# Kernel tuning notes

Measured on AMD Instinct MI355X. Metric: run time of the kernel, lower is better.

## Reference

```python
import jax, jax.numpy as jnp
import numpy as np
from jax import lax

N_STATES = 512
VOCAB = 32000
BATCH = 16
SEQ_LEN = 128


def setup_inputs() -> dict:
    key = jax.random.key(0)
    k_ids, k_em, k_tm, k_p = jax.random.split(key, 4)
    input_ids = jax.random.randint(k_ids, (BATCH, SEQ_LEN), 0, VOCAB, dtype=jnp.int64)
    em = jax.random.normal(k_em, (N_STATES, VOCAB), dtype=jnp.float32)
    tm = jax.random.normal(k_tm, (N_STATES, N_STATES), dtype=jnp.float32)
    p = jax.random.normal(k_p, (N_STATES,), dtype=jnp.float32)
    return {"input_ids": input_ids, "em": em, "tm": tm, "p": p}


def reference(input_ids, em, tm, p):
    """HMM forward algorithm in log space; returns mean NLL (scalar).

    em: [S, V] emission logits, tm: [S, S] transition logits, p: [S] prior logits.
    do_log_softmax=True -> normalize each in log space first.
    """
    log_em = jax.nn.log_softmax(em, axis=-1)   # [S, V]
    log_tm = jax.nn.log_softmax(tm, axis=-1)   # [S, S] rows = source state
    log_p = jax.nn.log_softmax(p, axis=-1)     # [S]

    # Gather emission log-probs per token: [B, T, S]
    em_tok = log_em.T[input_ids]

    # alpha_0[b, s] = log_p[s] + log_em[s, x_0]
    alpha0 = log_p[None, :] + em_tok[:, 0]     # [B, S]

    def step(alpha, e_t):
        # alpha: [B, S_src]; log-matmul: logsumexp over source states
        a = jax.nn.logsumexp(alpha[:, :, None] + log_tm[None, :, :], axis=1) + e_t
        return a, None

    em_rest = jnp.swapaxes(em_tok[:, 1:], 0, 1)  # [T-1, B, S]
    alpha_T, _ = lax.scan(step, alpha0, em_rest)

    # loss = -mean_b log p(x_b) = -mean_b logsumexp_s alpha_T[b, s]
    loss = -jnp.mean(jax.nn.logsumexp(alpha_T, axis=-1))
    return loss
```

## Files before the change

### kernel.cpp

```cpp
#include <hip/hip_runtime.h>
#include <hip/hip_bf16.h>

#define NS 512
#define NV 32000
#define NB 16
#define NT 128

#ifndef __has_builtin
#define __has_builtin(x) 0
#endif

typedef int v8i __attribute__((ext_vector_type(8)));
typedef float v4f __attribute__((ext_vector_type(4)));

__device__ inline unsigned enc_e4m3(float x) {
    x = fminf(x, 448.0f);
    unsigned u = __float_as_uint(x);
    if (x < 0.015625f) {
        return (unsigned)(int)rintf(x * 512.0f);
    }
    unsigned u2 = u + 0x7FFFFu + ((u >> 20) & 1u);
    return (((u2 >> 23) - 120u) << 3) | ((u2 >> 20) & 7u);
}

__device__ inline unsigned pack4_e4m3(float a, float b, float c, float d) {
#if __has_builtin(__builtin_amdgcn_cvt_pk_fp8_f32)
    int v = __builtin_amdgcn_cvt_pk_fp8_f32(a, b, 0, false);
    v = __builtin_amdgcn_cvt_pk_fp8_f32(c, d, v, true);
    return (unsigned)v;
#else
    return enc_e4m3(a) | (enc_e4m3(b) << 8) | (enc_e4m3(c) << 16) | (enc_e4m3(d) << 24);
#endif
}

__device__ inline unsigned pack1_e4m3(float a) {
#if __has_builtin(__builtin_amdgcn_cvt_pk_fp8_f32)
    return (unsigned)__builtin_amdgcn_cvt_pk_fp8_f32(a, 0.f, 0, false) & 0xFFFFu;
#else
    return enc_e4m3(a);
#endif
}

#define DPPMAX(x, ctrl) \
    x = fmaxf(x, __int_as_float(__builtin_amdgcn_mov_dpp(__float_as_int(x), ctrl, 0xF, 0xF, true)))
#define DPPADD(x, ctrl) \
    x = x + __int_as_float(__builtin_amdgcn_mov_dpp(__float_as_int(x), ctrl, 0xF, 0xF, true))

#define UMX(a, b) ((a) > (b) ? (a) : (b))

__device__ inline unsigned bytemax8(unsigned a, unsigned b) {
    unsigned m0 = UMX(a & 255u, b & 255u);
    unsigned m1 = UMX((a >> 8) & 255u, (b >> 8) & 255u);
    unsigned m2 = UMX((a >> 16) & 255u, (b >> 16) & 255u);
    unsigned m3 = UMX(a >> 24, b >> 24);
    return UMX(UMX(m0, m1), UMX(m2, m3));
}

__global__ __launch_bounds__(256) void k_emtok_T(
    const float* __restrict__ em, const int* __restrict__ ids,
    float* __restrict__ em_lin_T)
{
    const int s   = blockIdx.x;
    const int tid = threadIdx.x;
    const float* row = em + (size_t)s * NV;

    int idv[8];
#pragma unroll
    for (int k = 0; k < 8; ++k) idv[k] = ids[tid + 256 * k];
    float g[8];
#pragma unroll
    for (int k = 0; k < 8; ++k) g[k] = row[idv[k]];

    float sum = 0.f;
    const float4* row4 = (const float4*)row;
#pragma unroll 4
    for (int i = 0; i < 31; ++i) {
        float4 v = row4[tid + 256 * i];
        sum += __expf(v.x) + __expf(v.y) + __expf(v.z) + __expf(v.w);
    }
    sum += __expf(row[31744 + tid]);

#pragma unroll
    for (int off = 32; off; off >>= 1) sum += __shfl_down(sum, off);
    __shared__ float red[4];
    __shared__ float s_scale;
    if ((tid & 63) == 0) red[tid >> 6] = sum;
    __syncthreads();
    if (tid == 0) s_scale = (1.0f / ((red[0] + red[1]) + (red[2] + red[3]))) * 0x1p-18f;
    __syncthreads();
    const float scale = s_scale;

#pragma unroll
    for (int k = 0; k < 8; ++k)
        em_lin_T[(size_t)s * (NB * NT) + tid + 256 * k] = __expf(g[k]) * scale;
}

__global__ __launch_bounds__(256) void k_tr(
    const float* __restrict__ emT, float* __restrict__ em_lin)
{
    __shared__ float tile[32][33];
    const int jb = blockIdx.x * 32;
    const int sb = blockIdx.y * 32;
    const int cc = threadIdx.x & 31;
    const int rr = threadIdx.x >> 5;
#pragma unroll
    for (int i = 0; i < 4; ++i) {
        int r = rr + 8 * i;
        tile[r][cc] = emT[(size_t)(sb + r) * (NB * NT) + jb + cc];
    }
    __syncthreads();
#pragma unroll
    for (int i = 0; i < 4; ++i) {
        int r = rr + 8 * i;
        int s = sb + cc;
        int ps = (s & ~63) | ((s & 15) << 2) | ((s >> 4) & 3);
        em_lin[(size_t)(jb + r) * NS + ps] = tile[cc][r];
    }
}

__global__ __launch_bounds__(64) void k_z(
    const float* __restrict__ tm, float* __restrict__ zscale)
{
    const int k    = blockIdx.x;
    const int lane = threadIdx.x;
    const float* row = tm + (size_t)k * NS;

    float4 a = ((const float4*)row)[lane * 2];
    float4 b = ((const float4*)row)[lane * 2 + 1];
    float sum = ((__expf(a.x) + __expf(a.y)) + (__expf(a.z) + __expf(a.w)))
              + ((__expf(b.x) + __expf(b.y)) + (__expf(b.z) + __expf(b.w)));
#pragma unroll
    for (int off = 32; off; off >>= 1) sum += __shfl_down(sum, off);
    if (lane == 0) zscale[k] = 1024.0f / sum;
}

__global__ __launch_bounds__(256) void k_pt2(
    const float* __restrict__ tm, const float* __restrict__ zscale,
    unsigned char* __restrict__ PT)
{
    __shared__ float tile[64][65];
    __shared__ float zs[64];
    const int kb  = blockIdx.x * 64;
    const int db  = blockIdx.y * 64;
    const int tid = threadIdx.x;
    const int c   = tid & 63;
    const int r0  = tid >> 6;

    if (tid < 64) zs[tid] = zscale[kb + tid];
#pragma unroll
    for (int i = 0; i < 16; ++i) {
        int r = r0 + 4 * i;
        tile[r][c] = tm[(size_t)(kb + r) * NS + db + c];
    }
    __syncthreads();

    const int d  = tid >> 2;
    const int ks = (tid & 3) * 16;
    unsigned px[4];
#pragma unroll
    for (int gq = 0; gq < 4; ++gq) {
        int k0 = ks + gq * 4;
        px[gq] = pack4_e4m3(__expf(tile[k0 + 0][d]) * zs[k0 + 0],
                            __expf(tile[k0 + 1][d]) * zs[k0 + 1],
                            __expf(tile[k0 + 2][d]) * zs[k0 + 2],
                            __expf(tile[k0 + 3][d]) * zs[k0 + 3]);
    }
    uint4 o; o.x = px[0]; o.y = px[1]; o.z = px[2]; o.w = px[3];
    *(uint4*)(PT + (size_t)(db + d) * NS + kb + ks) = o;
}

__global__ __launch_bounds__(512, 2) void k_scan(
    const float* __restrict__ em_lin, const unsigned char* __restrict__ PT,
    const float* __restrict__ p, float* __restrict__ out)
{
    const int bb  = blockIdx.x;
    const int tid = threadIdx.x;
    const int w   = tid >> 6;
    const int l   = tid & 63;
    const int lc  = l & 15;
    const int lq  = l >> 4;

    __shared__ __align__(16) unsigned Ew[2][16 * 128];
    __shared__ __align__(4) unsigned char wmE2[2][32];
    __shared__ __align__(4) unsigned char mbuf[2][4];
    __shared__ float    wm2[8][4];
    __shared__ float    sbuf[4];

    v8i B[4][4];
#pragma unroll
    for (int nt = 0; nt < 4; ++nt) {
#pragma unroll
        for (int kt = 0; kt < 4; ++kt) {
            const uint4* src = (const uint4*)(PT + (size_t)((w * 4 + nt) * 16 + lc) * NS + kt * 128 + lq * 32);
            v8i bb8;
            *(uint4*)&bb8       = src[0];
            *((uint4*)&bb8 + 1) = src[1];
            B[nt][kt] = bb8;
        }
    }

    {
        uint4 zz; zz.x = 0; zz.y = 0; zz.z = 0; zz.w = 0;
        uint4* z = (uint4*)&Ew[0][0];
        z[tid * 2]     = zz;
        z[tid * 2 + 1] = zz;
    }

    float zp = 0.f;
#pragma unroll
    for (int i = 0; i < 8; ++i) zp += __expf(p[l * 8 + i]);
    DPPADD(zp, 0x128); DPPADD(zp, 0x124); DPPADD(zp, 0xB1); DPPADD(zp, 0x4E);
    float Zp = __int_as_float(__builtin_amdgcn_readlane(__float_as_int(zp), 0))
             + __int_as_float(__builtin_amdgcn_readlane(__float_as_int(zp), 16))
             + __int_as_float(__builtin_amdgcn_readlane(__float_as_int(zp), 32))
             + __int_as_float(__builtin_amdgcn_readlane(__float_as_int(zp), 48));
    const float invZp = 1.0f / Zp;

    const int dbase0 = w * 64 + lc;
    const int gb     = bb * 4 + lq;

    const float* epb0 = em_lin + (size_t)gb * (NT * NS) + (w * 64 + lc * 4);
    v4f e0 = *(const v4f*)epb0;
    float alpha[4];
#pragma unroll
    for (int nt = 0; nt < 4; ++nt)
        alpha[nt] = __expf(p[dbase0 + 16 * nt]) * invZp * e0[nt];

    int gsum = 18;
    const unsigned sel1 = (l & 1) ? 0x07030501u : 0x02060004u;
    const unsigned sel2 = (l & 2) ? 0x07060302u : 0x01000504u;
    const int mrow = 4 * lq + (l & 3);

    int aidx[8];
#pragma unroll
    for (int kt = 0; kt < 4; ++kt) {
#pragma unroll
        for (int c = 0; c < 2; ++c)
            aidx[kt * 2 + c] = lc * 32 + (((kt * 8 + lq * 2 + c) ^ lc) & 31);
    }
    int widx[4];
#pragma unroll
    for (int nt = 0; nt < 4; ++nt)
        widx[nt] = mrow * 128 + ((((w * 4 + nt) ^ mrow) & 31) << 2) + (lc >> 2);

    const int bA = lc >> 2;
    const int h  = lq >> 1;
    const int wexp_w = (w & 1) * 16 + lq * 4 + (w >> 1);
    const int wexp_r = h * 16 + bA * 4;
    const unsigned shA = (unsigned)(bA << 3);
    const unsigned shQ = (unsigned)(lq << 3);
    const bool real = (l & 3) == 0;

    const float* epb = epb0 + NS;

    {
        float mx = fmaxf(fmaxf(alpha[0], alpha[1]), fmaxf(alpha[2], alpha[3]));
        DPPMAX(mx, 0x128); DPPMAX(mx, 0x124); DPPMAX(mx, 0xB1); DPPMAX(mx, 0x4E);
        unsigned E = __float_as_uint(mx) >> 23;
        E = E > 1u ? E : 1u;
        if (lc == 0) wmE2[1][wexp_w] = (unsigned char)E;
    }
    __syncthreads();
    if (tid < 4) {
        const unsigned u0 = *(const unsigned*)&wmE2[1][tid * 4];
        const unsigned u1 = *(const unsigned*)&wmE2[1][16 + tid * 4];
        mbuf[1][tid] = (unsigned char)bytemax8(u0, u1);
    }

    const v4f CZ = {0.f, 0.f, 0.f, 0.f};

    v8i A[4];
#pragma unroll
    for (int kt = 0; kt < 4; ++kt)
#pragma unroll
        for (int i = 0; i < 8; ++i) A[kt][i] = 0;

    for (int t = 1; t < NT; ++t) {
        const int buf = t & 1;
        unsigned* EwB = &Ew[buf][0];

        float mx = fmaxf(fmaxf(alpha[0], alpha[1]), fmaxf(alpha[2], alpha[3]));
        DPPMAX(mx, 0x128); DPPMAX(mx, 0x124); DPPMAX(mx, 0xB1); DPPMAX(mx, 0x4E);
        unsigned E = __float_as_uint(mx) >> 23;
        E = E > 1u ? E : 1u;
        const float sc = __uint_as_float((261u - E) << 23);

        unsigned dwv[4];
#pragma unroll
        for (int nt = 0; nt < 4; ++nt) {
            unsigned dw = pack1_e4m3(alpha[nt] * sc);
            int tmp = __builtin_amdgcn_mov_dpp((int)dw, 0xB1, 0xF, 0xF, true);
            dw = __builtin_amdgcn_perm(dw, (unsigned)tmp, sel1);
            tmp = __builtin_amdgcn_mov_dpp((int)dw, 0x4E, 0xF, 0xF, true);
            dw = __builtin_amdgcn_perm(dw, (unsigned)tmp, sel2);
            dwv[nt] = dw;
        }
        if (real) {
#pragma unroll
            for (int nt = 0; nt < 4; ++nt) EwB[widx[nt]] = dwv[nt];
        }
        if (lc == 0) wmE2[buf][wexp_w] = (unsigned char)E;
        __syncthreads();

        const unsigned dwE = *(const unsigned*)&wmE2[buf][wexp_r];
        const unsigned mdw = *(const unsigned*)&mbuf[buf][0];

        v4f epf = *(const v4f*)epb;
        epb += NS;

        if (real) {
            const uint4* eb4 = (const uint4*)EwB;
#pragma unroll
            for (int kt = 0; kt < 4; ++kt) {
                *(uint4*)&A[kt]       = eb4[aidx[kt * 2 + 0]];
                *((uint4*)&A[kt] + 1) = eb4[aidx[kt * 2 + 1]];
            }
        }

        const int MhA = (int)((mdw >> shA) & 255u);
        const int MhQ = (int)((mdw >> shQ) & 255u);
        gsum += MhQ - 126;

        const int base = 127 - MhA;
        int s0 = (int)(dwE & 255u) + base;         s0 = s0 < 0 ? 0 : (s0 > 254 ? 254 : s0);
        int s1 = (int)((dwE >> 8) & 255u) + base;  s1 = s1 < 0 ? 0 : (s1 > 254 ? 254 : s1);
        int s2 = (int)((dwE >> 16) & 255u) + base; s2 = s2 < 0 ? 0 : (s2 > 254 ? 254 : s2);
        int s3 = (int)(dwE >> 24) + base;          s3 = s3 < 0 ? 0 : (s3 > 254 ? 254 : s3);
        const int scA[4] = { s0 * 0x01010101, s1 * 0x01010101,
                             s2 * 0x01010101, s3 * 0x01010101 };

        v4f Ca[4], Cb[4];
#pragma unroll
        for (int nt = 0; nt < 4; ++nt)
            Ca[nt] = __builtin_amdgcn_mfma_scale_f32_16x16x128_f8f6f4(
                         A[0], B[nt][0], CZ, 0, 0, 0, scA[0], 0, 0x7F7F7F7F);
#pragma unroll
        for (int nt = 0; nt < 4; ++nt)
            Ca[nt] = __builtin_amdgcn_mfma_scale_f32_16x16x128_f8f6f4(
                         A[1], B[nt][1], Ca[nt], 0, 0, 0, scA[1], 0, 0x7F7F7F7F);
#pragma unroll
        for (int nt = 0; nt < 4; ++nt)
            Cb[nt] = __builtin_amdgcn_mfma_scale_f32_16x16x128_f8f6f4(
                         A[2], B[nt][2], CZ, 0, 0, 0, scA[2], 0, 0x7F7F7F7F);
#pragma unroll
        for (int nt = 0; nt < 4; ++nt)
            Cb[nt] = __builtin_amdgcn_mfma_scale_f32_16x16x128_f8f6f4(
                         A[3], B[nt][3], Cb[nt], 0, 0, 0, scA[3], 0, 0x7F7F7F7F);

        if (tid < 4) {
            const unsigned u0 = *(const unsigned*)&wmE2[buf][tid * 4];
            const unsigned u1 = *(const unsigned*)&wmE2[buf][16 + tid * 4];
            mbuf[buf ^ 1][tid] = (unsigned char)bytemax8(u0, u1);
        }

#pragma unroll
        for (int nt = 0; nt < 4; ++nt)
            alpha[nt] = (Ca[nt][0] + Cb[nt][0]) * epf[nt];
    }

    {
        float sm = (alpha[0] + alpha[1]) + (alpha[2] + alpha[3]);
        DPPADD(sm, 0x128); DPPADD(sm, 0x124); DPPADD(sm, 0xB1); DPPADD(sm, 0x4E);
        if (lc == 0) wm2[w][lq] = sm;
        if (w == 0 && lc == 0) sbuf[lq] = (float)gsum;
    }
    __syncthreads();
    if (tid < 4) {
        float s8 = ((wm2[0][tid] + wm2[1][tid]) + (wm2[2][tid] + wm2[3][tid]))
                 + ((wm2[4][tid] + wm2[5][tid]) + (wm2[6][tid] + wm2[7][tid]));
        float L2 = __log2f(s8) + sbuf[tid];
        atomicAdd(out, -(0.693147180559945f / 16.0f) * L2);
    }
}

extern "C" void kernel_launch(void* const* d_in, const int* in_sizes, int n_in,
                              void* d_out, int out_size, void* d_ws, size_t ws_size,
                              hipStream_t stream)
{
    const int*   ids = (const int*)d_in[0];
    const float* em  = (const float*)d_in[1];
    const float* tm  = (const float*)d_in[2];
    const float* p   = (const float*)d_in[3];
    float* out = (float*)d_out;

    float*          em_lin = (float*)d_ws;
    unsigned char*  PT     = (unsigned char*)d_ws + ((size_t)4 << 20);
    float*          zscale = (float*)((unsigned char*)d_ws + ((size_t)4 << 20) + ((size_t)256 << 10));
    float*          emT    = (float*)((unsigned char*)d_ws + ((size_t)4 << 20) + ((size_t)512 << 10));

    hipMemsetAsync(d_out, 0, sizeof(float), stream);

    k_emtok_T<<<NS, 256, 0, stream>>>(em, ids, emT);
    k_tr<<<dim3(64, 16), 256, 0, stream>>>(emT, em_lin);
    k_z<<<NS, 64, 0, stream>>>(tm, zscale);
    k_pt2<<<dim3(8, 8), 256, 0, stream>>>(tm, zscale, PT);
    k_scan<<<4, 512, 0, stream>>>(em_lin, PT, p, out);
}
```

Before: 248.3 us.

## Fuse emission gather into scan kernel and merge transition preprocessing kernels

Drops the separate emission gather/transpose kernels: the scan kernel now reads raw emission logits per token directly from em, prefetching one step ahead, and applies exp with a per-state inverse normalizer computed by a reduced k_logz kernel. The transition normalizer and the fp8 pack are merged into one kernel that loops over destination blocks. The per-step block max is now computed redundantly in each lane from shared memory instead of by a separate mbuf stage. This cuts the launch count and intermediate traffic, but adds scattered global loads and exps on the serial scan path, and the merged transition kernel runs on only 8 blocks.

```diff
diff --git a/kernel.cpp b/kernel.cpp
--- a/kernel.cpp
+++ b/kernel.cpp
@@ -56,20 +56,12 @@
     return UMX(UMX(m0, m1), UMX(m2, m3));
 }
 
-__global__ __launch_bounds__(256) void k_emtok_T(
-    const float* __restrict__ em, const int* __restrict__ ids,
-    float* __restrict__ em_lin_T)
+__global__ __launch_bounds__(256) void k_logz(
+    const float* __restrict__ em, float* __restrict__ invZs)
 {
     const int s   = blockIdx.x;
     const int tid = threadIdx.x;
     const float* row = em + (size_t)s * NV;
-
-    int idv[8];
-#pragma unroll
-    for (int k = 0; k < 8; ++k) idv[k] = ids[tid + 256 * k];
-    float g[8];
-#pragma unroll
-    for (int k = 0; k < 8; ++k) g[k] = row[idv[k]];
 
     float sum = 0.f;
     const float4* row4 = (const float4*)row;
@@ -83,94 +75,66 @@
 #pragma unroll
     for (int off = 32; off; off >>= 1) sum += __shfl_down(sum, off);
     __shared__ float red[4];
-    __shared__ float s_scale;
     if ((tid & 63) == 0) red[tid >> 6] = sum;
     __syncthreads();
-    if (tid == 0) s_scale = (1.0f / ((red[0] + red[1]) + (red[2] + red[3]))) * 0x1p-18f;
-    __syncthreads();
-    const float scale = s_scale;
-
-#pragma unroll
-    for (int k = 0; k < 8; ++k)
-        em_lin_T[(size_t)s * (NB * NT) + tid + 256 * k] = __expf(g[k]) * scale;
-}
-
-__global__ __launch_bounds__(256) void k_tr(
-    const float* __restrict__ emT, float* __restrict__ em_lin)
-{
-    __shared__ float tile[32][33];
-    const int jb = blockIdx.x * 32;
-    const int sb = blockIdx.y * 32;
-    const int cc = threadIdx.x & 31;
-    const int rr = threadIdx.x >> 5;
-#pragma unroll
-    for (int i = 0; i < 4; ++i) {
-        int r = rr + 8 * i;
-        tile[r][cc] = emT[(size_t)(sb + r) * (NB * NT) + jb + cc];
-    }
-    __syncthreads();
-#pragma unroll
-    for (int i = 0; i < 4; ++i) {
-        int r = rr + 8 * i;
-        int s = sb + cc;
-        int ps = (s & ~63) | ((s & 15) << 2) | ((s >> 4) & 3);
-        em_lin[(size_t)(jb + r) * NS + ps] = tile[cc][r];
-    }
-}
-
-__global__ __launch_bounds__(64) void k_z(
-    const float* __restrict__ tm, float* __restrict__ zscale)
-{
-    const int k    = blockIdx.x;
-    const int lane = threadIdx.x;
-    const float* row = tm + (size_t)k * NS;
-
-    float4 a = ((const float4*)row)[lane * 2];
-    float4 b = ((const float4*)row)[lane * 2 + 1];
-    float sum = ((__expf(a.x) + __expf(a.y)) + (__expf(a.z) + __expf(a.w)))
-              + ((__expf(b.x) + __expf(b.y)) + (__expf(b.z) + __expf(b.w)));
-#pragma unroll
-    for (int off = 32; off; off >>= 1) sum += __shfl_down(sum, off);
-    if (lane == 0) zscale[k] = 1024.0f / sum;
-}
-
-__global__ __launch_bounds__(256) void k_pt2(
-    const float* __restrict__ tm, const float* __restrict__ zscale,
-    unsigned char* __restrict__ PT)
+    if (tid == 0)
+        invZs[s] = (1.0f / ((red[0] + red[1]) + (red[2] + red[3]))) * 0x1p-18f;
+}
+
+__global__ __launch_bounds__(256) void k_pt2f(
+    const float* __restrict__ tm, unsigned char* __restrict__ PT)
 {
     __shared__ float tile[64][65];
     __shared__ float zs[64];
+    __shared__ float part[64][4];
     const int kb  = blockIdx.x * 64;
-    const int db  = blockIdx.y * 64;
     const int tid = threadIdx.x;
-    const int c   = tid & 63;
-    const int r0  = tid >> 6;
-
-    if (tid < 64) zs[tid] = zscale[kb + tid];
-#pragma unroll
-    for (int i = 0; i < 16; ++i) {
-        int r = r0 + 4 * i;
-        tile[r][c] = tm[(size_t)(kb + r) * NS + db + c];
-    }
-    __syncthreads();
-
+
+    {
+        const int r = tid >> 2, q = tid & 3;
+        const float4* rp = (const float4*)(tm + (size_t)(kb + r) * NS + q * 128);
+        float s = 0.f;
+#pragma unroll 8
+        for (int i = 0; i < 32; ++i) {
+            float4 v = rp[i];
+            s += (__expf(v.x) + __expf(v.y)) + (__expf(v.z) + __expf(v.w));
+        }
+        part[r][q] = s;
+    }
+    __syncthreads();
+    if (tid < 64)
+        zs[tid] = 1024.0f / ((part[tid][0] + part[tid][1]) + (part[tid][2] + part[tid][3]));
+    __syncthreads();
+
+    const int c  = tid & 63;
+    const int r0 = tid >> 6;
     const int d  = tid >> 2;
     const int ks = (tid & 3) * 16;
-    unsigned px[4];
-#pragma unroll
-    for (int gq = 0; gq < 4; ++gq) {
-        int k0 = ks + gq * 4;
-        px[gq] = pack4_e4m3(__expf(tile[k0 + 0][d]) * zs[k0 + 0],
-                            __expf(tile[k0 + 1][d]) * zs[k0 + 1],
-                            __expf(tile[k0 + 2][d]) * zs[k0 + 2],
-                            __expf(tile[k0 + 3][d]) * zs[k0 + 3]);
-    }
-    uint4 o; o.x = px[0]; o.y = px[1]; o.z = px[2]; o.w = px[3];
-    *(uint4*)(PT + (size_t)(db + d) * NS + kb + ks) = o;
+    for (int db = 0; db < NS; db += 64) {
+#pragma unroll
+        for (int i = 0; i < 16; ++i) {
+            int r = r0 + 4 * i;
+            tile[r][c] = tm[(size_t)(kb + r) * NS + db + c];
+        }
+        __syncthreads();
+        unsigned px[4];
+#pragma unroll
+        for (int gq = 0; gq < 4; ++gq) {
+            int k0 = ks + gq * 4;
+            px[gq] = pack4_e4m3(__expf(tile[k0 + 0][d]) * zs[k0 + 0],
+                                __expf(tile[k0 + 1][d]) * zs[k0 + 1],
+                                __expf(tile[k0 + 2][d]) * zs[k0 + 2],
+                                __expf(tile[k0 + 3][d]) * zs[k0 + 3]);
+        }
+        uint4 o; o.x = px[0]; o.y = px[1]; o.z = px[2]; o.w = px[3];
+        *(uint4*)(PT + (size_t)(db + d) * NS + kb + ks) = o;
+        __syncthreads();
+    }
 }
 
 __global__ __launch_bounds__(512, 2) void k_scan(
-    const float* __restrict__ em_lin, const unsigned char* __restrict__ PT,
+    const float* __restrict__ em, const int* __restrict__ ids,
+    const float* __restrict__ invZs, const unsigned char* __restrict__ PT,
     const float* __restrict__ p, float* __restrict__ out)
 {
     const int bb  = blockIdx.x;
@@ -182,7 +146,6 @@
 
     __shared__ __align__(16) unsigned Ew[2][16 * 128];
     __shared__ __align__(4) unsigned char wmE2[2][32];
-    __shared__ __align__(4) unsigned char mbuf[2][4];
     __shared__ float    wm2[8][4];
     __shared__ float    sbuf[4];
 
@@ -219,12 +182,22 @@
     const int dbase0 = w * 64 + lc;
     const int gb     = bb * 4 + lq;
 
-    const float* epb0 = em_lin + (size_t)gb * (NT * NS) + (w * 64 + lc * 4);
-    v4f e0 = *(const v4f*)epb0;
+    const int* idp = ids + gb * NT;
+    const float* er[4];
+    float iz[4];
+#pragma unroll
+    for (int nt = 0; nt < 4; ++nt) {
+        er[nt] = em + (size_t)(dbase0 + 16 * nt) * NV;
+        iz[nt] = invZs[dbase0 + 16 * nt];
+    }
+
     float alpha[4];
-#pragma unroll
-    for (int nt = 0; nt < 4; ++nt)
-        alpha[nt] = __expf(p[dbase0 + 16 * nt]) * invZp * e0[nt];
+    {
+        const int id0 = idp[0];
+#pragma unroll
+        for (int nt = 0; nt < 4; ++nt)
+            alpha[nt] = __expf(p[dbase0 + 16 * nt]) * invZp * (__expf(er[nt][id0]) * iz[nt]);
+    }
 
     int gsum = 18;
     const unsigned sel1 = (l & 1) ? 0x07030501u : 0x02060004u;
@@ -246,26 +219,9 @@
     const int bA = lc >> 2;
     const int h  = lq >> 1;
     const int wexp_w = (w & 1) * 16 + lq * 4 + (w >> 1);
-    const int wexp_r = h * 16 + bA * 4;
-    const unsigned shA = (unsigned)(bA << 3);
-    const unsigned shQ = (unsigned)(lq << 3);
     const bool real = (l & 3) == 0;
 
-    const float* epb = epb0 + NS;
-
-    {
-        float mx = fmaxf(fmaxf(alpha[0], alpha[1]), fmaxf(alpha[2], alpha[3]));
-        DPPMAX(mx, 0x128); DPPMAX(mx, 0x124); DPPMAX(mx, 0xB1); DPPMAX(mx, 0x4E);
-        unsigned E = __float_as_uint(mx) >> 23;
-        E = E > 1u ? E : 1u;
-        if (lc == 0) wmE2[1][wexp_w] = (unsigned char)E;
-    }
-    __syncthreads();
-    if (tid < 4) {
-        const unsigned u0 = *(const unsigned*)&wmE2[1][tid * 4];
-        const unsigned u1 = *(const unsigned*)&wmE2[1][16 + tid * 4];
-        mbuf[1][tid] = (unsigned char)bytemax8(u0, u1);
-    }
+    __syncthreads();
 
     const v4f CZ = {0.f, 0.f, 0.f, 0.f};
 
@@ -274,6 +230,15 @@
     for (int kt = 0; kt < 4; ++kt)
 #pragma unroll
         for (int i = 0; i < 8; ++i) A[kt][i] = 0;
+
+    float gcur[4];
+    int idB;
+    {
+        const int idA = idp[1];
+#pragma unroll
+        for (int nt = 0; nt < 4; ++nt) gcur[nt] = er[nt][idA];
+        idB = idp[2];
+    }
 
     for (int t = 1; t < NT; ++t) {
         const int buf = t & 1;
@@ -302,11 +267,15 @@
         if (lc == 0) wmE2[buf][wexp_w] = (unsigned char)E;
         __syncthreads();
 
-        const unsigned dwE = *(const unsigned*)&wmE2[buf][wexp_r];
-        const unsigned mdw = *(const unsigned*)&mbuf[buf][0];
-
-        v4f epf = *(const v4f*)epb;
-        epb += NS;
+        const unsigned dA0 = *(const unsigned*)&wmE2[buf][bA * 4];
+        const unsigned dA1 = *(const unsigned*)&wmE2[buf][16 + bA * 4];
+        const unsigned dQ0 = *(const unsigned*)&wmE2[buf][lq * 4];
+        const unsigned dQ1 = *(const unsigned*)&wmE2[buf][16 + lq * 4];
+
+        float gnxt[4];
+#pragma unroll
+        for (int nt = 0; nt < 4; ++nt) gnxt[nt] = er[nt][idB];
+        idB = idp[(t + 2) & 127];
 
         if (real) {
             const uint4* eb4 = (const uint4*)EwB;
@@ -317,15 +286,16 @@
             }
         }
 
-        const int MhA = (int)((mdw >> shA) & 255u);
-        const int MhQ = (int)((mdw >> shQ) & 255u);
-        gsum += MhQ - 126;
-
-        const int base = 127 - MhA;
-        int s0 = (int)(dwE & 255u) + base;         s0 = s0 < 0 ? 0 : (s0 > 254 ? 254 : s0);
-        int s1 = (int)((dwE >> 8) & 255u) + base;  s1 = s1 < 0 ? 0 : (s1 > 254 ? 254 : s1);
-        int s2 = (int)((dwE >> 16) & 255u) + base; s2 = s2 < 0 ? 0 : (s2 > 254 ? 254 : s2);
-        int s3 = (int)(dwE >> 24) + base;          s3 = s3 < 0 ? 0 : (s3 > 254 ? 254 : s3);
+        const unsigned MA = bytemax8(dA0, dA1);
+        const unsigned MQ = bytemax8(dQ0, dQ1);
+        gsum += (int)MQ - 126;
+
+        const unsigned dwE = h ? dA1 : dA0;
+        const int base = 127 - (int)MA;
+        int s0 = (int)(dwE & 255u) + base;         s0 = s0 < 0 ? 0 : s0;
+        int s1 = (int)((dwE >> 8) & 255u) + base;  s1 = s1 < 0 ? 0 : s1;
+        int s2 = (int)((dwE >> 16) & 255u) + base; s2 = s2 < 0 ? 0 : s2;
+        int s3 = (int)(dwE >> 24) + base;          s3 = s3 < 0 ? 0 : s3;
         const int scA[4] = { s0 * 0x01010101, s1 * 0x01010101,
                              s2 * 0x01010101, s3 * 0x01010101 };
 
@@ -347,15 +317,11 @@
             Cb[nt] = __builtin_amdgcn_mfma_scale_f32_16x16x128_f8f6f4(
                          A[3], B[nt][3], Cb[nt], 0, 0, 0, scA[3], 0, 0x7F7F7F7F);
 
-        if (tid < 4) {
-            const unsigned u0 = *(const unsigned*)&wmE2[buf][tid * 4];
-            const unsigned u1 = *(const unsigned*)&wmE2[buf][16 + tid * 4];
-            mbuf[buf ^ 1][tid] = (unsigned char)bytemax8(u0, u1);
-        }
-
-#pragma unroll
-        for (int nt = 0; nt < 4; ++nt)
-            alpha[nt] = (Ca[nt][0] + Cb[nt][0]) * epf[nt];
+#pragma unroll
+        for (int nt = 0; nt < 4; ++nt)
+            alpha[nt] = (Ca[nt][0] + Cb[nt][0]) * (__expf(gcur[nt]) * iz[nt]);
+#pragma unroll
+        for (int nt = 0; nt < 4; ++nt) gcur[nt] = gnxt[nt];
     }
 
     {
@@ -383,16 +349,12 @@
     const float* p   = (const float*)d_in[3];
     float* out = (float*)d_out;
 
-    float*          em_lin = (float*)d_ws;
-    unsigned char*  PT     = (unsigned char*)d_ws + ((size_t)4 << 20);
-    float*          zscale = (float*)((unsigned char*)d_ws + ((size_t)4 << 20) + ((size_t)256 << 10));
-    float*          emT    = (float*)((unsigned char*)d_ws + ((size_t)4 << 20) + ((size_t)512 << 10));
+    float*          invZs = (float*)d_ws;
+    unsigned char*  PT    = (unsigned char*)d_ws + ((size_t)64 << 10);
 
     hipMemsetAsync(d_out, 0, sizeof(float), stream);
 
-    k_emtok_T<<<NS, 256, 0, stream>>>(em, ids, emT);
-    k_tr<<<dim3(64, 16), 256, 0, stream>>>(emT, em_lin);
-    k_z<<<NS, 64, 0, stream>>>(tm, zscale);
-    k_pt2<<<dim3(8, 8), 256, 0, stream>>>(tm, zscale, PT);
-    k_scan<<<4, 512, 0, stream>>>(em_lin, PT, p, out);
-}
+    k_logz<<<NS, 256, 0, stream>>>(em, invZs);
+    k_pt2f<<<8, 256, 0, stream>>>(tm, PT);
+    k_scan<<<4, 512, 0, stream>>>(em, ids, invZs, PT, p, out);
+}
```

Measured after the change: 500.5 us. 2.02x slower.
